# Kernel optimization log

Measured on AMD Instinct MI355X. Metric: run time of the kernel, lower is better.

## Reference

```python
import jax, jax.numpy as jnp
import numpy as np

N, E, D, O = 50000, 800000, 128, 128
BN_EPS = 1e-5

def setup_inputs() -> dict:
    key = jax.random.key(0)
    ks = jax.random.split(key, 12)
    s1 = 1.0 / np.sqrt(D)
    s2 = 1.0 / np.sqrt(O)
    return {
        "x": jax.random.normal(ks[0], (N, D), dtype=jnp.float32),
        "edge_index": jax.random.randint(ks[1], (2, E), 0, N, dtype=jnp.int64),
        "batch": jnp.zeros((N,), dtype=jnp.int64),
        "eps": jnp.float32(0.0),  # GINConv train_eps parameter, init 0
        "W1": jax.random.uniform(ks[2], (O, D), jnp.float32, -s1, s1),
        "b1": jax.random.uniform(ks[3], (O,), jnp.float32, -s1, s1),
        "gamma1": jnp.ones((O,), jnp.float32),
        "beta1": jnp.zeros((O,), jnp.float32),
        "W2": jax.random.uniform(ks[4], (O, O), jnp.float32, -s2, s2),
        "b2": jax.random.uniform(ks[5], (O,), jnp.float32, -s2, s2),
        "gamma2": jnp.ones((O,), jnp.float32),
        "beta2": jnp.zeros((O,), jnp.float32),
    }

def _bn(h, gamma, beta):
    # BatchNorm1d training mode: biased variance over nodes
    m = jnp.mean(h, axis=0)
    v = jnp.var(h, axis=0)
    return (h - m) * jax.lax.rsqrt(v + BN_EPS) * gamma + beta

def reference(x, edge_index, batch, eps, W1, b1, gamma1, beta1, W2, b2, gamma2, beta2):
    src, dst = edge_index[0], edge_index[1]
    # sum_{j in N(i)} x_j  (scatter-add over edges)
    agg = jax.ops.segment_sum(x[src], dst, num_segments=N)
    h = (1.0 + eps) * x + agg
    h = jax.nn.relu(_bn(h @ W1.T + b1, gamma1, beta1))
    h = jax.nn.relu(_bn(h @ W2.T + b2, gamma2, beta2))
    return h
```

## Files before the change

### kernel.cpp

```cpp
#include <hip/hip_runtime.h>
#include <hip/hip_bf16.h>

typedef __hip_bfloat16 bf16;
typedef unsigned short u16;
typedef unsigned int u32;
typedef __attribute__((ext_vector_type(8))) short short8;
typedef __attribute__((ext_vector_type(4))) float floatx4;

#define N_NODES 50000
#define N_EDGES 800000
#define DIM 128
#define NBUCK 391
#define CAP 2560
#define T_EDGES 8192

__device__ __forceinline__ u16 f2bfbits(float f) {
    bf16 h = __float2bfloat16(f);
    return *(u16*)&h;
}
__device__ __forceinline__ unsigned pack2(float a, float b) {
    return (unsigned)f2bfbits(a) | ((unsigned)f2bfbits(b) << 16);
}
__device__ __forceinline__ float lo2f(u32 u) { u32 v = u << 16; return __builtin_bit_cast(float, v); }
__device__ __forceinline__ float hi2f(u32 u) { u32 v = u & 0xFFFF0000u; return __builtin_bit_cast(float, v); }
__device__ __forceinline__ float b162f(u16 u) { u32 v = (u32)u << 16; return __builtin_bit_cast(float, v); }

__global__ void prep_kernel(const float* __restrict__ x, u32* __restrict__ xb,
                            const int* __restrict__ ei, int* __restrict__ flags,
                            int* __restrict__ gcur, float* __restrict__ stats) {
    int t = threadIdx.x;
    if (blockIdx.x == 0) {
        if (t < NBUCK) gcur[t] = 0;
        if (t + 256 < NBUCK) gcur[t + 256] = 0;
        stats[t] = 0.f; stats[t + 256] = 0.f;
        if (t == 0) {
            int acc = 0;
            for (int k = 0; k < 64; k++) acc |= ei[2 * k + 1];
            flags[1] = (acc == 0) ? 1 : 0;
        }
    }
    int i = (blockIdx.x * 256 + t) * 8;
    floatx4 v0 = *(const floatx4*)&x[i];
    floatx4 v1 = *(const floatx4*)&x[i + 4];
    uint4 r;
    r.x = pack2(v0[0], v0[1]); r.y = pack2(v0[2], v0[3]);
    r.z = pack2(v1[0], v1[1]); r.w = pack2(v1[2], v1[3]);
    *(uint4*)&xb[i / 2] = r;
}

__launch_bounds__(256)
__global__ void sort1_kernel(const int* __restrict__ ei, const int* __restrict__ flags,
                             u32* __restrict__ gbuck, int* __restrict__ gcur) {
    __shared__ int hist[512];
    __shared__ int offs[512];
    __shared__ int partial[256];
    __shared__ int cur[NBUCK];
    __shared__ int gbase[NBUCK];
    __shared__ u32 buf[T_EDGES];
    int t = threadIdx.x;
    int is64 = flags[1];
    int e0 = blockIdx.x * T_EDGES;
    int n = N_EDGES - e0; if (n > T_EDGES) n = T_EDGES;

    for (int i = t; i < 512; i += 256) hist[i] = 0;
    for (int i = t; i < NBUCK; i += 256) cur[i] = 0;
    __syncthreads();

    u32 ed[T_EDGES / 256];
    #pragma unroll
    for (int j = 0; j < T_EDGES / 256; j++) {
        int idx = j * 256 + t;
        if (idx < n) {
            int e = e0 + idx;
            int js = e, jd = N_EDGES + e;
            if (is64) { js = 2 * e; jd = 2 * (N_EDGES + e); }
            u32 p = (u32)ei[js] | ((u32)ei[jd] << 16);
            ed[j] = p;
            atomicAdd(&hist[p >> 23], 1);
        }
    }
    __syncthreads();

    int a0 = hist[2 * t], a1 = hist[2 * t + 1];
    partial[t] = a0 + a1;
    __syncthreads();
    for (int d = 1; d < 256; d <<= 1) {
        int v = (t >= d) ? partial[t - d] : 0;
        __syncthreads();
        partial[t] += v;
        __syncthreads();
    }
    int ex = partial[t] - (a0 + a1);
    offs[2 * t] = ex; offs[2 * t + 1] = ex + a0;
    __syncthreads();

    #pragma unroll
    for (int j = 0; j < T_EDGES / 256; j++) {
        int idx = j * 256 + t;
        if (idx < n) {
            int b = ed[j] >> 23;
            int s = offs[b] + atomicAdd(&cur[b], 1);
            buf[s] = ed[j];
        }
    }
    for (int i = t; i < NBUCK; i += 256) {
        int c = hist[i];
        gbase[i] = c ? atomicAdd(&gcur[i], c) : 0;
    }
    __syncthreads();

    int wv = t >> 6, lane = t & 63;
    for (int b = wv; b < NBUCK; b += 4) {
        int c = hist[b], o = offs[b];
        long gb = (long)b * CAP + gbase[b];
        for (int j = lane; j < c; j += 64) gbuck[gb + j] = buf[o + j];
    }
}

__launch_bounds__(256)
__global__ void sort2_kernel(const u32* __restrict__ gbuck, const int* __restrict__ gcur,
                             u32* __restrict__ nbrs, int* __restrict__ starts,
                             int* __restrict__ counts) {
    __shared__ int cnt[128];
    __shared__ int offs[128];
    __shared__ int cur[128];
    __shared__ u32 buf[CAP];
    __shared__ u32 buf2[CAP];
    int b = blockIdx.x, t = threadIdx.x;
    int n = gcur[b];
    long base = (long)b * CAP;
    if (t < 128) { cnt[t] = 0; cur[t] = 0; }
    __syncthreads();

    for (int i = t; i < n; i += 256) {
        u32 p = gbuck[base + i];
        buf[i] = p;
        atomicAdd(&cnt[(p >> 16) & 127], 1);
    }
    __syncthreads();

    if (t < 128) offs[t] = cnt[t];
    __syncthreads();
    for (int d = 1; d < 128; d <<= 1) {
        int v = 0;
        if (t < 128 && t >= d) v = offs[t - d];
        __syncthreads();
        if (t < 128) offs[t] += v;
        __syncthreads();
    }
    if (t < 128) offs[t] -= cnt[t];
    __syncthreads();

    for (int i = t; i < n; i += 256) {
        u32 p = buf[i];
        int d = (p >> 16) & 127;
        int s = offs[d] + atomicAdd(&cur[d], 1);
        buf2[s] = p & 0xFFFF;
    }
    __syncthreads();

    for (int i = t; i < n; i += 256) nbrs[base + i] = buf2[i];
    if (t < 128) {
        starts[b * 128 + t] = (int)(base + offs[t]);
        counts[b * 128 + t] = cnt[t];
    }
}

__global__ void agg_kernel(const u32* __restrict__ xb, const int* __restrict__ starts,
                           const int* __restrict__ counts, const u32* __restrict__ nbrs,
                           const float* __restrict__ epsp, u32* __restrict__ hw) {
    int lane = threadIdx.x & 63;
    int node = blockIdx.x * 4 + (threadIdx.x >> 6);
    float ep1 = 1.0f + epsp[0];
    u32 self = xb[node * 64 + lane];
    float ax = ep1 * lo2f(self), ay = ep1 * hi2f(self);
    int s = starts[node], e = s + counts[node];
    int i = s;
    for (; i + 16 <= e; i += 16) {
        int nn[16];
        u32 u[16];
        #pragma unroll
        for (int j = 0; j < 16; j++) nn[j] = nbrs[i + j];
        #pragma unroll
        for (int j = 0; j < 16; j++) u[j] = xb[nn[j] * 64 + lane];
        #pragma unroll
        for (int j = 0; j < 16; j++) { ax += lo2f(u[j]); ay += hi2f(u[j]); }
    }
    for (; i + 8 <= e; i += 8) {
        int nn[8];
        u32 u[8];
        #pragma unroll
        for (int j = 0; j < 8; j++) nn[j] = nbrs[i + j];
        #pragma unroll
        for (int j = 0; j < 8; j++) u[j] = xb[nn[j] * 64 + lane];
        #pragma unroll
        for (int j = 0; j < 8; j++) { ax += lo2f(u[j]); ay += hi2f(u[j]); }
    }
    for (; i + 2 <= e; i += 2) {
        u32 u0 = xb[nbrs[i] * 64 + lane], u1 = xb[nbrs[i + 1] * 64 + lane];
        ax += lo2f(u0) + lo2f(u1); ay += hi2f(u0) + hi2f(u1);
    }
    if (i < e) {
        u32 u = xb[nbrs[i] * 64 + lane];
        ax += lo2f(u); ay += hi2f(u);
    }
    hw[node * 64 + lane] = pack2(ax, ay);
}

template<int TRANSFORM>
__launch_bounds__(256)
__global__ void gemm_mfma(const u16* __restrict__ Ap, const float* __restrict__ Wp,
                          const float* __restrict__ bias,
                          const float* __restrict__ gamma, const float* __restrict__ beta,
                          const float* __restrict__ gsum, const float* __restrict__ gsq,
                          u16* __restrict__ Yp, float* __restrict__ osum, float* __restrict__ osq) {
    __shared__ u16 sW[128 * 136];
    __shared__ float sScale[128], sShift[128], sBias[128], sSum[128], sSq[128];
    int t = threadIdx.x, lane = t & 63, wv = t >> 6;

    #pragma unroll
    for (int it = 0; it < 16; it++) {
        int q = it * 256 + t;
        int r = q >> 5, cq = q & 31;
        floatx4 w = ((const floatx4*)Wp)[q];
        u16 bb[4] = {f2bfbits(w[0]), f2bfbits(w[1]), f2bfbits(w[2]), f2bfbits(w[3])};
        *(uint2*)&sW[r * 136 + cq * 4] = *(uint2*)bb;
    }
    if (t < 128) {
        sSum[t] = 0.f; sSq[t] = 0.f; sBias[t] = bias[t];
        if (TRANSFORM) {
            float m = gsum[t] * (1.0f / N_NODES);
            float v = fmaxf(gsq[t] * (1.0f / N_NODES) - m * m, 0.0f);
            float rs = rsqrtf(v + 1e-5f);
            float sc = gamma[t] * rs;
            sScale[t] = sc;
            sShift[t] = beta[t] - m * sc;
        }
    }
    __syncthreads();

    int tile = blockIdx.x * 4 + wv;
    if (tile < (N_NODES / 16)) {
        int col0 = lane & 15, quad = lane >> 4;
        int mrow = tile * 16 + col0;

        short8 afr[4];
        #pragma unroll
        for (int ks = 0; ks < 4; ks++) {
            int kb = ks * 32 + quad * 8;
            short8 a = *(const short8*)&Ap[mrow * DIM + kb];
            if (TRANSFORM) {
                short8 r;
                #pragma unroll
                for (int j = 0; j < 8; j++) {
                    float f = b162f((u16)a[j]);
                    r[j] = (short)f2bfbits(fmaxf(fmaf(f, sScale[kb + j], sShift[kb + j]), 0.f));
                }
                afr[ks] = r;
            } else {
                afr[ks] = a;
            }
        }

        floatx4 acc[8];
        #pragma unroll
        for (int nt = 0; nt < 8; nt++) acc[nt] = (floatx4){0.f, 0.f, 0.f, 0.f};
        #pragma unroll
        for (int ks = 0; ks < 4; ks++) {
            #pragma unroll
            for (int nt = 0; nt < 8; nt++) {
                short8 bfr = *(const short8*)&sW[(nt * 16 + col0) * 136 + ks * 32 + quad * 8];
                acc[nt] = __builtin_amdgcn_mfma_f32_16x16x32_bf16(afr[ks], bfr, acc[nt], 0, 0, 0);
            }
        }

        #pragma unroll
        for (int nt = 0; nt < 8; nt++) {
            int col = nt * 16 + col0;
            float bb = sBias[col];
            float o0 = acc[nt][0] + bb, o1 = acc[nt][1] + bb;
            float o2 = acc[nt][2] + bb, o3 = acc[nt][3] + bb;
            int rbase = tile * 16 + quad * 4;
            Yp[(rbase + 0) * DIM + col] = f2bfbits(o0);
            Yp[(rbase + 1) * DIM + col] = f2bfbits(o1);
            Yp[(rbase + 2) * DIM + col] = f2bfbits(o2);
            Yp[(rbase + 3) * DIM + col] = f2bfbits(o3);
            float s = o0 + o1 + o2 + o3;
            float q = o0 * o0 + o1 * o1 + o2 * o2 + o3 * o3;
            s += __shfl_xor(s, 16); s += __shfl_xor(s, 32);
            q += __shfl_xor(q, 16); q += __shfl_xor(q, 32);
            if (quad == 0) { atomicAdd(&sSum[col], s); atomicAdd(&sSq[col], q); }
        }
    }
    __syncthreads();
    if (t < 128) { atomicAdd(&osum[t], sSum[t]); atomicAdd(&osq[t], sSq[t]); }
}

__global__ void output_kernel(const u32* __restrict__ Y,
                              const float* __restrict__ gsum, const float* __restrict__ gsq,
                              const float* __restrict__ gamma, const float* __restrict__ beta,
                              float* __restrict__ out) {
    __shared__ float sScale[128], sShift[128];
    int t = threadIdx.x;
    if (t < 128) {
        float m = gsum[t] * (1.0f / N_NODES);
        float v = fmaxf(gsq[t] * (1.0f / N_NODES) - m * m, 0.0f);
        float rs = rsqrtf(v + 1e-5f);
        float sc = gamma[t] * rs;
        sScale[t] = sc;
        sShift[t] = beta[t] - m * sc;
    }
    __syncthreads();
    int i = (blockIdx.x * 256 + t) * 8;
    int c = i & 127;
    uint4 v = *(const uint4*)&Y[i / 2];
    u32 w[4] = {v.x, v.y, v.z, v.w};
    floatx4 o0, o1;
    #pragma unroll
    for (int j = 0; j < 4; j++) {
        float lo = lo2f(w[j]), hi = hi2f(w[j]);
        float r0 = fmaxf(fmaf(lo, sScale[c + 2 * j],     sShift[c + 2 * j]),     0.f);
        float r1 = fmaxf(fmaf(hi, sScale[c + 2 * j + 1], sShift[c + 2 * j + 1]), 0.f);
        if (j < 2) { o0[2 * j] = r0; o0[2 * j + 1] = r1; }
        else       { o1[2 * (j - 2)] = r0; o1[2 * (j - 2) + 1] = r1; }
    }
    *(floatx4*)&out[i] = o0;
    *(floatx4*)&out[i + 4] = o1;
}

extern "C" void kernel_launch(void* const* d_in, const int* in_sizes, int n_in,
                              void* d_out, int out_size, void* d_ws, size_t ws_size,
                              hipStream_t stream) {
    const float* x   = (const float*)d_in[0];
    const int* eraw  = (const int*)d_in[1];
    const float* eps = (const float*)d_in[3];
    const float* W1  = (const float*)d_in[4];
    const float* b1  = (const float*)d_in[5];
    const float* g1  = (const float*)d_in[6];
    const float* be1 = (const float*)d_in[7];
    const float* W2  = (const float*)d_in[8];
    const float* b2  = (const float*)d_in[9];
    const float* g2  = (const float*)d_in[10];
    const float* be2 = (const float*)d_in[11];

    char* ws = (char*)d_ws;
    size_t off = 0;
    u32* xb = (u32*)(ws + off);          off += (size_t)N_NODES * DIM * 2;
    u32* h1 = (u32*)(ws + off);          off += (size_t)N_NODES * DIM * 2;
    u16* y1 = (u16*)(ws + off);          off += (size_t)N_NODES * DIM * 2;
    u16* y2 = (u16*)(ws + off);          off += (size_t)N_NODES * DIM * 2;
    float* stats = (float*)(ws + off);   off += 4 * 128 * 4;
    float* sum1 = stats, *sq1 = stats + 128, *sum2 = stats + 256, *sq2 = stats + 384;
    u32* gbuck = (u32*)(ws + off);       off += (size_t)NBUCK * CAP * 4;
    u32* nbrs = (u32*)(ws + off);        off += (size_t)NBUCK * CAP * 4;
    int* starts = (int*)(ws + off);      off += (size_t)NBUCK * 128 * 4;
    int* counts = (int*)(ws + off);      off += (size_t)NBUCK * 128 * 4;
    int* gcur = (int*)(ws + off);        off += 512 * 4;
    int* flags = (int*)(ws + off);       off += 16 * 4;

    prep_kernel<<<N_NODES * DIM / (8 * 256), 256, 0, stream>>>(x, xb, eraw, flags, gcur, stats);
    sort1_kernel<<<(N_EDGES + T_EDGES - 1) / T_EDGES, 256, 0, stream>>>(eraw, flags, gbuck, gcur);
    sort2_kernel<<<NBUCK, 256, 0, stream>>>(gbuck, gcur, nbrs, starts, counts);
    agg_kernel<<<N_NODES / 4, 256, 0, stream>>>(xb, starts, counts, nbrs, eps, h1);

    const int gemmGrid = (N_NODES / 16 + 3) / 4;
    gemm_mfma<0><<<gemmGrid, 256, 0, stream>>>((const u16*)h1, W1, b1,
                                               nullptr, nullptr, nullptr, nullptr, y1, sum1, sq1);
    gemm_mfma<1><<<gemmGrid, 256, 0, stream>>>(y1, W2, b2,
                                               g1, be1, sum1, sq1, y2, sum2, sq2);
    output_kernel<<<N_NODES * DIM / (8 * 256), 256, 0, stream>>>((const u32*)y2, sum2, sq2,
                                                                 g2, be2, (float*)d_out);
}
```

Baseline: 234.2 us.

## Replace two-pass edge sort with atomic bucket fill and fused sort-aggregate kernel

Drops the block-local histogram sort and the separate second sort pass. Edges now go straight into 1563 buckets of 32 destination nodes each via global atomics. A single kernel then sorts each bucket by destination in shared memory and immediately gathers neighbor features for its 32 nodes, which removes the nbrs/starts/counts round trip through global memory and one kernel launch. This relies on heavy global atomic contention per bucket, and bucket capacity is clamped at 768, which could silently drop edges if a bucket overflows.

```diff
diff --git a/kernel.cpp b/kernel.cpp
--- a/kernel.cpp
+++ b/kernel.cpp
@@ -10,9 +10,8 @@
 #define N_NODES 50000
 #define N_EDGES 800000
 #define DIM 128
-#define NBUCK 391
-#define CAP 2560
-#define T_EDGES 8192
+#define NB2 1563
+#define CAP2 768
 
 __device__ __forceinline__ u16 f2bfbits(float f) {
     bf16 h = __float2bfloat16(f);
@@ -30,8 +29,11 @@
                             int* __restrict__ gcur, float* __restrict__ stats) {
     int t = threadIdx.x;
     if (blockIdx.x == 0) {
-        if (t < NBUCK) gcur[t] = 0;
-        if (t + 256 < NBUCK) gcur[t + 256] = 0;
+        #pragma unroll
+        for (int j = 0; j < 7; j++) {
+            int i = j * 256 + t;
+            if (i < NB2) gcur[i] = 0;
+        }
         stats[t] = 0.f; stats[t + 256] = 0.f;
         if (t == 0) {
             int acc = 0;
@@ -48,163 +50,91 @@
     *(uint4*)&xb[i / 2] = r;
 }
 
-__launch_bounds__(256)
-__global__ void sort1_kernel(const int* __restrict__ ei, const int* __restrict__ flags,
-                             u32* __restrict__ gbuck, int* __restrict__ gcur) {
-    __shared__ int hist[512];
-    __shared__ int offs[512];
-    __shared__ int partial[256];
-    __shared__ int cur[NBUCK];
-    __shared__ int gbase[NBUCK];
-    __shared__ u32 buf[T_EDGES];
-    int t = threadIdx.x;
+__global__ void fill_kernel(const int* __restrict__ ei, const int* __restrict__ flags,
+                            u32* __restrict__ gbuck, int* __restrict__ gcur) {
     int is64 = flags[1];
-    int e0 = blockIdx.x * T_EDGES;
-    int n = N_EDGES - e0; if (n > T_EDGES) n = T_EDGES;
-
-    for (int i = t; i < 512; i += 256) hist[i] = 0;
-    for (int i = t; i < NBUCK; i += 256) cur[i] = 0;
-    __syncthreads();
-
-    u32 ed[T_EDGES / 256];
+    int base = blockIdx.x * 1024 + threadIdx.x;
     #pragma unroll
-    for (int j = 0; j < T_EDGES / 256; j++) {
-        int idx = j * 256 + t;
-        if (idx < n) {
-            int e = e0 + idx;
+    for (int j = 0; j < 4; j++) {
+        int e = base + j * 256;
+        if (e < N_EDGES) {
             int js = e, jd = N_EDGES + e;
             if (is64) { js = 2 * e; jd = 2 * (N_EDGES + e); }
             u32 p = (u32)ei[js] | ((u32)ei[jd] << 16);
-            ed[j] = p;
-            atomicAdd(&hist[p >> 23], 1);
-        }
-    }
-    __syncthreads();
-
-    int a0 = hist[2 * t], a1 = hist[2 * t + 1];
-    partial[t] = a0 + a1;
-    __syncthreads();
-    for (int d = 1; d < 256; d <<= 1) {
-        int v = (t >= d) ? partial[t - d] : 0;
-        __syncthreads();
-        partial[t] += v;
-        __syncthreads();
-    }
-    int ex = partial[t] - (a0 + a1);
-    offs[2 * t] = ex; offs[2 * t + 1] = ex + a0;
-    __syncthreads();
-
-    #pragma unroll
-    for (int j = 0; j < T_EDGES / 256; j++) {
-        int idx = j * 256 + t;
-        if (idx < n) {
-            int b = ed[j] >> 23;
-            int s = offs[b] + atomicAdd(&cur[b], 1);
-            buf[s] = ed[j];
-        }
-    }
-    for (int i = t; i < NBUCK; i += 256) {
-        int c = hist[i];
-        gbase[i] = c ? atomicAdd(&gcur[i], c) : 0;
-    }
-    __syncthreads();
-
-    int wv = t >> 6, lane = t & 63;
-    for (int b = wv; b < NBUCK; b += 4) {
-        int c = hist[b], o = offs[b];
-        long gb = (long)b * CAP + gbase[b];
-        for (int j = lane; j < c; j += 64) gbuck[gb + j] = buf[o + j];
+            int b = p >> 21;
+            int pos = atomicAdd(&gcur[b], 1);
+            gbuck[(long)b * CAP2 + pos] = p;
+        }
     }
 }
 
 __launch_bounds__(256)
-__global__ void sort2_kernel(const u32* __restrict__ gbuck, const int* __restrict__ gcur,
-                             u32* __restrict__ nbrs, int* __restrict__ starts,
-                             int* __restrict__ counts) {
-    __shared__ int cnt[128];
-    __shared__ int offs[128];
-    __shared__ int cur[128];
-    __shared__ u32 buf[CAP];
-    __shared__ u32 buf2[CAP];
-    int b = blockIdx.x, t = threadIdx.x;
-    int n = gcur[b];
-    long base = (long)b * CAP;
-    if (t < 128) { cnt[t] = 0; cur[t] = 0; }
-    __syncthreads();
-
+__global__ void sortagg_kernel(const u32* __restrict__ xb, const u32* __restrict__ gbuck,
+                               const int* __restrict__ gcur, const float* __restrict__ epsp,
+                               u32* __restrict__ hw) {
+    __shared__ u32 sbuf[CAP2];
+    __shared__ u16 slist[CAP2];
+    __shared__ int cnt[32], offs[32], cur[32];
+    int t = threadIdx.x, lane = t & 63, wv = t >> 6;
+    int b = blockIdx.x;
+    int n = gcur[b]; if (n > CAP2) n = CAP2;
+    long base = (long)b * CAP2;
+
+    if (t < 32) { cnt[t] = 0; cur[t] = 0; }
+    __syncthreads();
     for (int i = t; i < n; i += 256) {
         u32 p = gbuck[base + i];
-        buf[i] = p;
-        atomicAdd(&cnt[(p >> 16) & 127], 1);
-    }
-    __syncthreads();
-
-    if (t < 128) offs[t] = cnt[t];
-    __syncthreads();
-    for (int d = 1; d < 128; d <<= 1) {
-        int v = 0;
-        if (t < 128 && t >= d) v = offs[t - d];
-        __syncthreads();
-        if (t < 128) offs[t] += v;
-        __syncthreads();
-    }
-    if (t < 128) offs[t] -= cnt[t];
-    __syncthreads();
-
+        sbuf[i] = p;
+        atomicAdd(&cnt[(p >> 16) & 31], 1);
+    }
+    __syncthreads();
+    if (t < 32) {
+        int v = cnt[t];
+        int pv = v;
+        #pragma unroll
+        for (int d = 1; d < 32; d <<= 1) {
+            int up = __shfl_up(pv, d);
+            if (t >= d) pv += up;
+        }
+        offs[t] = pv - v;
+    }
+    __syncthreads();
     for (int i = t; i < n; i += 256) {
-        u32 p = buf[i];
-        int d = (p >> 16) & 127;
-        int s = offs[d] + atomicAdd(&cur[d], 1);
-        buf2[s] = p & 0xFFFF;
-    }
-    __syncthreads();
-
-    for (int i = t; i < n; i += 256) nbrs[base + i] = buf2[i];
-    if (t < 128) {
-        starts[b * 128 + t] = (int)(base + offs[t]);
-        counts[b * 128 + t] = cnt[t];
-    }
-}
-
-__global__ void agg_kernel(const u32* __restrict__ xb, const int* __restrict__ starts,
-                           const int* __restrict__ counts, const u32* __restrict__ nbrs,
-                           const float* __restrict__ epsp, u32* __restrict__ hw) {
-    int lane = threadIdx.x & 63;
-    int node = blockIdx.x * 4 + (threadIdx.x >> 6);
+        u32 p = sbuf[i];
+        int d = (p >> 16) & 31;
+        int pos = offs[d] + atomicAdd(&cur[d], 1);
+        slist[pos] = (u16)(p & 0xFFFF);
+    }
+    __syncthreads();
+
     float ep1 = 1.0f + epsp[0];
-    u32 self = xb[node * 64 + lane];
-    float ax = ep1 * lo2f(self), ay = ep1 * hi2f(self);
-    int s = starts[node], e = s + counts[node];
-    int i = s;
-    for (; i + 16 <= e; i += 16) {
-        int nn[16];
-        u32 u[16];
-        #pragma unroll
-        for (int j = 0; j < 16; j++) nn[j] = nbrs[i + j];
-        #pragma unroll
-        for (int j = 0; j < 16; j++) u[j] = xb[nn[j] * 64 + lane];
-        #pragma unroll
-        for (int j = 0; j < 16; j++) { ax += lo2f(u[j]); ay += hi2f(u[j]); }
-    }
-    for (; i + 8 <= e; i += 8) {
-        int nn[8];
-        u32 u[8];
-        #pragma unroll
-        for (int j = 0; j < 8; j++) nn[j] = nbrs[i + j];
-        #pragma unroll
-        for (int j = 0; j < 8; j++) u[j] = xb[nn[j] * 64 + lane];
-        #pragma unroll
-        for (int j = 0; j < 8; j++) { ax += lo2f(u[j]); ay += hi2f(u[j]); }
-    }
-    for (; i + 2 <= e; i += 2) {
-        u32 u0 = xb[nbrs[i] * 64 + lane], u1 = xb[nbrs[i + 1] * 64 + lane];
-        ax += lo2f(u0) + lo2f(u1); ay += hi2f(u0) + hi2f(u1);
-    }
-    if (i < e) {
-        u32 u = xb[nbrs[i] * 64 + lane];
-        ax += lo2f(u); ay += hi2f(u);
-    }
-    hw[node * 64 + lane] = pack2(ax, ay);
+    for (int nn = wv; nn < 32; nn += 4) {
+        int node = b * 32 + nn;
+        if (node >= N_NODES) break;
+        u32 self = xb[node * 64 + lane];
+        float ax = ep1 * lo2f(self), ay = ep1 * hi2f(self);
+        int s = offs[nn], e = s + cnt[nn];
+        int i = s;
+        for (; i + 8 <= e; i += 8) {
+            int m[8];
+            u32 u[8];
+            #pragma unroll
+            for (int j = 0; j < 8; j++) m[j] = slist[i + j];
+            #pragma unroll
+            for (int j = 0; j < 8; j++) u[j] = xb[m[j] * 64 + lane];
+            #pragma unroll
+            for (int j = 0; j < 8; j++) { ax += lo2f(u[j]); ay += hi2f(u[j]); }
+        }
+        for (; i + 2 <= e; i += 2) {
+            u32 u0 = xb[(int)slist[i] * 64 + lane], u1 = xb[(int)slist[i + 1] * 64 + lane];
+            ax += lo2f(u0) + lo2f(u1); ay += hi2f(u0) + hi2f(u1);
+        }
+        if (i < e) {
+            u32 u = xb[(int)slist[i] * 64 + lane];
+            ax += lo2f(u); ay += hi2f(u);
+        }
+        hw[node * 64 + lane] = pack2(ax, ay);
+    }
 }
 
 template<int TRANSFORM>
@@ -351,17 +281,13 @@
     u16* y2 = (u16*)(ws + off);          off += (size_t)N_NODES * DIM * 2;
     float* stats = (float*)(ws + off);   off += 4 * 128 * 4;
     float* sum1 = stats, *sq1 = stats + 128, *sum2 = stats + 256, *sq2 = stats + 384;
-    u32* gbuck = (u32*)(ws + off);       off += (size_t)NBUCK * CAP * 4;
-    u32* nbrs = (u32*)(ws + off);        off += (size_t)NBUCK * CAP * 4;
-    int* starts = (int*)(ws + off);      off += (size_t)NBUCK * 128 * 4;
-    int* counts = (int*)(ws + off);      off += (size_t)NBUCK * 128 * 4;
-    int* gcur = (int*)(ws + off);        off += 512 * 4;
+    u32* gbuck = (u32*)(ws + off);       off += (size_t)NB2 * CAP2 * 4;
+    int* gcur = (int*)(ws + off);        off += (size_t)((NB2 + 255) & ~255) * 4;
     int* flags = (int*)(ws + off);       off += 16 * 4;
 
     prep_kernel<<<N_NODES * DIM / (8 * 256), 256, 0, stream>>>(x, xb, eraw, flags, gcur, stats);
-    sort1_kernel<<<(N_EDGES + T_EDGES - 1) / T_EDGES, 256, 0, stream>>>(eraw, flags, gbuck, gcur);
-    sort2_kernel<<<NBUCK, 256, 0, stream>>>(gbuck, gcur, nbrs, starts, counts);
-    agg_kernel<<<N_NODES / 4, 256, 0, stream>>>(xb, starts, counts, nbrs, eps, h1);
+    fill_kernel<<<(N_EDGES + 1023) / 1024, 256, 0, stream>>>(eraw, flags, gbuck, gcur);
+    sortagg_kernel<<<NB2, 256, 0, stream>>>(xb, gbuck, gcur, eps, h1);
 
     const int gemmGrid = (N_NODES / 16 + 3) / 4;
     gemm_mfma<0><<<gemmGrid, 256, 0, stream>>>((const u16*)h1, W1, b1,
```

New measurement: 317.6 us. 1.36x slower.
